# Kernel optimization log

Hardware: AMD Instinct MI355X
Metric: run time of the kernel (lower is better)

The kernel has to match this reference:

```python
import jax, jax.numpy as jnp
import numpy as np
import math

IN_DIM = 256
HID_DIM = 256
NUM_EDGE_TYPES = 3
HEADS = 8
HEAD_DIM = HID_DIM // HEADS  # 32
QK_DIM = (NUM_EDGE_TYPES + 1) * HID_DIM  # 1024
N = 4096


def _glorot(key, shape):
    # torch_geometric-style glorot: uniform(-a, a), a = sqrt(6/(fan_in+fan_out)) over last two dims
    a = math.sqrt(6.0 / (shape[-2] + shape[-1]))
    return jax.random.uniform(key, shape, jnp.float32, -a, a)


def setup_inputs() -> dict:
    key = jax.random.key(0)
    ks = jax.random.split(key, 8)
    return {
        "input_x": jax.random.normal(ks[0], (N, IN_DIM), jnp.float32),
        "pe_Q": jax.random.normal(ks[1], (N, NUM_EDGE_TYPES * HID_DIM), jnp.float32),
        "pe_K": jax.random.normal(ks[2], (N, NUM_EDGE_TYPES * HID_DIM), jnp.float32),
        "A": jnp.zeros((N, N), jnp.int32),  # accepted by forward but unused
        "WQ": _glorot(ks[3], (HEADS, QK_DIM, HEAD_DIM)),
        "WK": _glorot(ks[4], (HEADS, QK_DIM, HEAD_DIM)),
        "WV": _glorot(ks[5], (HEADS, IN_DIM, HEAD_DIM)),
        "Q_bias": jnp.zeros((HEADS, 1, HEAD_DIM), jnp.float32),
        "K_bias": jnp.zeros((HEADS, 1, HEAD_DIM), jnp.float32),
        "V_bias": jnp.zeros((HEADS, 1, HEAD_DIM), jnp.float32),
        "lin_w": _glorot(ks[6], (HID_DIM, HID_DIM)),
        "lin_b": jnp.zeros((HID_DIM,), jnp.float32),
    }


def reference(input_x, pe_Q, pe_K, A, WQ, WK, WV, Q_bias, K_bias, V_bias, lin_w, lin_b):
    x_Q = jnp.concatenate([input_x, pe_Q], axis=-1)  # [N, QK_DIM]
    x_K = jnp.concatenate([input_x, pe_K], axis=-1)  # [N, QK_DIM]
    Q = jnp.einsum('nd,hdk->hnk', x_Q, WQ) + Q_bias   # [H, N, hd]
    K = jnp.einsum('nd,hdk->hnk', x_K, WK) + K_bias   # [H, N, hd]
    V = jnp.einsum('nd,hdk->hnk', input_x, WV) + V_bias
    scores = jnp.einsum('hnk,hmk->hnm', Q, K) / math.sqrt(HID_DIM)  # [H, N, N]
    scores = scores - jax.lax.stop_gradient(jnp.max(scores, axis=-1, keepdims=True))
    attn = jax.nn.softmax(scores, axis=-1)
    attn = jnp.where(jnp.isnan(attn), jnp.zeros_like(attn), attn)
    attn_x = jnp.einsum('hnm,hmk->hnk', attn, V)      # [H, N, hd]
    # cat(list over heads, dim=1) -> [N, H*hd] with head-major column order
    x_cat = jnp.transpose(attn_x, (1, 0, 2)).reshape(attn_x.shape[1], -1)
    return x_cat @ lin_w.T + lin_b
```

## Files before the change

kernel.cpp:

```cpp
#include <hip/hip_runtime.h>
#include <hip/hip_bf16.h>

typedef __attribute__((ext_vector_type(8))) short bf16x8;
typedef __attribute__((ext_vector_type(4))) float f32x4;

#define QSCALE 0.09016844f

__device__ __forceinline__ unsigned short f2b(float f) {
    union { float f; unsigned int u; } v; v.f = f;
    unsigned int u = v.u;
    unsigned int r = (u + 0x7FFFu + ((u >> 16) & 1u)) >> 16;
    return (unsigned short)r;
}
__device__ __forceinline__ float b2f(unsigned short h) {
    union { unsigned int u; float f; } v; v.u = ((unsigned int)h) << 16;
    return v.f;
}
__device__ __forceinline__ unsigned pk2(float a, float b) {
    union { __hip_bfloat162 h; unsigned u; } c;
    c.h = __float22bfloat162_rn(make_float2(a, b));
    return c.u;
}

__global__ __launch_bounds__(256) void prep_main(
    const float* __restrict__ WQ, const float* __restrict__ WK,
    const float* __restrict__ WV, const float* __restrict__ LW,
    const float* __restrict__ Qb, const float* __restrict__ Kb,
    const float* __restrict__ Vb,
    const float* __restrict__ x, const float* __restrict__ peQ,
    const float* __restrict__ peK,
    unsigned short* __restrict__ WQt, unsigned short* __restrict__ WKt,
    unsigned short* __restrict__ WVt, unsigned short* __restrict__ LWt,
    unsigned short* __restrict__ Bq, unsigned short* __restrict__ Bk,
    unsigned short* __restrict__ Bv,
    unsigned short* __restrict__ xb, unsigned short* __restrict__ peQb,
    unsigned short* __restrict__ peKb) {
    int b = blockIdx.x, t = threadIdx.x;
    if (b < 288) {
        const float* W; unsigned short* Wt; int h, d0, D; float sc = 1.0f;
        if (b < 128)      { W = WQ; Wt = WQt; h = b >> 4;   d0 = (b & 15) * 64; D = 1024; sc = QSCALE; }
        else if (b < 256) { int bb = b - 128; W = WK; Wt = WKt; h = bb >> 4; d0 = (bb & 15) * 64; D = 1024; }
        else              { int bb = b - 256; W = WV; Wt = WVt; h = bb >> 2; d0 = (bb & 3) * 64;  D = 256; }
        __shared__ float Ts[32][65];
        int dr = t >> 2, k0 = (t & 3) * 8;
        const float* src = W + (h * D + d0 + dr) * 32 + k0;
        float4 u0 = *(const float4*)src;
        float4 u1 = *(const float4*)(src + 4);
        Ts[k0 + 0][dr] = u0.x; Ts[k0 + 1][dr] = u0.y; Ts[k0 + 2][dr] = u0.z; Ts[k0 + 3][dr] = u0.w;
        Ts[k0 + 4][dr] = u1.x; Ts[k0 + 5][dr] = u1.y; Ts[k0 + 6][dr] = u1.z; Ts[k0 + 7][dr] = u1.w;
        __syncthreads();
        int k = t >> 3, dc = (t & 7) * 8;
        union { unsigned short s[8]; uint4 v; } pk;
#pragma unroll
        for (int i = 0; i < 8; i++) pk.s[i] = f2b(Ts[k][dc + i] * sc);
        *(uint4*)(Wt + (h * 32 + k) * D + d0 + dc) = pk.v;
    } else if (b < 320) {
        int base = (b - 288) * 2048 + t * 8;
        const float* sp = LW + base;
        float4 u0 = *(const float4*)sp;
        float4 u1 = *(const float4*)(sp + 4);
        union { unsigned u[4]; uint4 v; } pk;
        pk.u[0] = pk2(u0.x, u0.y); pk.u[1] = pk2(u0.z, u0.w);
        pk.u[2] = pk2(u1.x, u1.y); pk.u[3] = pk2(u1.z, u1.w);
        *(uint4*)(LWt + base) = pk.v;
    } else if (b == 320) {
        Bq[t] = f2b(Qb[t] * QSCALE); Bk[t] = f2b(Kb[t]); Bv[t] = f2b(Vb[t]);
    } else {
        int idx = (b - 321) * 2048 + t * 8;
        const float* sp; unsigned short* dp;
        if (idx < 1048576)      { sp = x + idx;                dp = xb + idx; }
        else if (idx < 4194304) { sp = peQ + (idx - 1048576);  dp = peQb + (idx - 1048576); }
        else                    { sp = peK + (idx - 4194304);  dp = peKb + (idx - 4194304); }
        float4 u0 = *(const float4*)sp;
        float4 u1 = *(const float4*)(sp + 4);
        union { unsigned u[4]; uint4 v; } pk;
        pk.u[0] = pk2(u0.x, u0.y); pk.u[1] = pk2(u0.z, u0.w);
        pk.u[2] = pk2(u1.x, u1.y); pk.u[3] = pk2(u1.z, u1.w);
        *(uint4*)dp = pk.v;
    }
}

__global__ __launch_bounds__(256) void prep_fb(
    const float* __restrict__ WQ, const float* __restrict__ WK,
    const float* __restrict__ WV,
    const float* __restrict__ Qb, const float* __restrict__ Kb,
    const float* __restrict__ Vb,
    unsigned short* __restrict__ WQt, unsigned short* __restrict__ WKt,
    unsigned short* __restrict__ WVt,
    unsigned short* __restrict__ Bq, unsigned short* __restrict__ Bk,
    unsigned short* __restrict__ Bv) {
    int b = blockIdx.x, t = threadIdx.x;
    if (b < 288) {
        const float* W; unsigned short* Wt; int h, d0, D; float sc = 1.0f;
        if (b < 128)      { W = WQ; Wt = WQt; h = b >> 4;   d0 = (b & 15) * 64; D = 1024; sc = QSCALE; }
        else if (b < 256) { int bb = b - 128; W = WK; Wt = WKt; h = bb >> 4; d0 = (bb & 15) * 64; D = 1024; }
        else              { int bb = b - 256; W = WV; Wt = WVt; h = bb >> 2; d0 = (bb & 3) * 64;  D = 256; }
        __shared__ float Ts[32][65];
        int dr = t >> 2, k0 = (t & 3) * 8;
        const float* src = W + (h * D + d0 + dr) * 32 + k0;
        float4 u0 = *(const float4*)src;
        float4 u1 = *(const float4*)(src + 4);
        Ts[k0 + 0][dr] = u0.x; Ts[k0 + 1][dr] = u0.y; Ts[k0 + 2][dr] = u0.z; Ts[k0 + 3][dr] = u0.w;
        Ts[k0 + 4][dr] = u1.x; Ts[k0 + 5][dr] = u1.y; Ts[k0 + 6][dr] = u1.z; Ts[k0 + 7][dr] = u1.w;
        __syncthreads();
        int k = t >> 3, dc = (t & 7) * 8;
        union { unsigned short s[8]; uint4 v; } pk;
#pragma unroll
        for (int i = 0; i < 8; i++) pk.s[i] = f2b(Ts[k][dc + i] * sc);
        *(uint4*)(Wt + (h * 32 + k) * D + d0 + dc) = pk.v;
    } else {
        Bq[t] = f2b(Qb[t] * QSCALE); Bk[t] = f2b(Kb[t]); Bv[t] = f2b(Vb[t]);
    }
}

template <bool ABF16>
__global__ __launch_bounds__(256) void proj_fused(
    const void* __restrict__ xv,
    const void* __restrict__ peQv, const void* __restrict__ peKv,
    const unsigned short* __restrict__ WQt, const unsigned short* __restrict__ WKt,
    const unsigned short* __restrict__ WVt,
    const unsigned short* __restrict__ Bq, const unsigned short* __restrict__ Bk,
    const unsigned short* __restrict__ Bv,
    unsigned short* __restrict__ Qc, unsigned short* __restrict__ KV) {
    __shared__ unsigned short As[64 * 72];
    __shared__ unsigned short Bs[64 * 72];
    int bx = blockIdx.x;
    int which = bx >> 8, bb = bx & 255;
    const void* A1; const unsigned short* Bt; const unsigned short* bias; int K;
    if (which == 0)      { A1 = peQv; Bt = WQt; bias = Bq; K = 1024; }
    else if (which == 1) { A1 = peKv; Bt = WKt; bias = Bk; K = 1024; }
    else                 { A1 = peQv; Bt = WVt; bias = Bv; K = 256; }
    int mb = bb & 63, nb = bb >> 6;
    int m0 = mb * 64, n0 = nb * 64;
    int t = threadIdx.x, w = t >> 6, lane = t & 63;
    int ln = lane & 15, q8 = (lane >> 4) * 8;
    int wm = (w >> 1) * 32, wn = (w & 1) * 32;
    int sr = t >> 3, sc = (t & 7) * 8;
    f32x4 acc[2][2];
#pragma unroll
    for (int i = 0; i < 2; i++)
#pragma unroll
        for (int j = 0; j < 2; j++) acc[i][j] = (f32x4){0.f, 0.f, 0.f, 0.f};
    for (int kb = 0; kb < K; kb += 64) {
#pragma unroll
        for (int half = 0; half < 2; half++) {
            int r = sr + half * 32;
            int c = kb + sc;
            if (ABF16) {
                const unsigned short* ap = (c < 256)
                    ? ((const unsigned short*)xv + (m0 + r) * 256 + c)
                    : ((const unsigned short*)A1 + (m0 + r) * 768 + (c - 256));
                *(uint4*)&As[r * 72 + sc] = *(const uint4*)ap;
            } else {
                const float* ap = (c < 256)
                    ? ((const float*)xv + (m0 + r) * 256 + c)
                    : ((const float*)A1 + (m0 + r) * 768 + (c - 256));
                float4 u0 = *(const float4*)ap;
                float4 u1 = *(const float4*)(ap + 4);
                union { unsigned u[4]; uint4 v; } pk;
                pk.u[0] = pk2(u0.x, u0.y); pk.u[1] = pk2(u0.z, u0.w);
                pk.u[2] = pk2(u1.x, u1.y); pk.u[3] = pk2(u1.z, u1.w);
                *(uint4*)&As[r * 72 + sc] = pk.v;
            }
            *(uint4*)&Bs[r * 72 + sc] = *(const uint4*)(Bt + (n0 + r) * K + c);
        }
        __syncthreads();
#pragma unroll
        for (int ks = 0; ks < 64; ks += 32) {
            bf16x8 a[2], b[2];
#pragma unroll
            for (int i = 0; i < 2; i++) {
                a[i] = *(const bf16x8*)&As[(wm + i * 16 + ln) * 72 + ks + q8];
                b[i] = *(const bf16x8*)&Bs[(wn + i * 16 + ln) * 72 + ks + q8];
            }
#pragma unroll
            for (int i = 0; i < 2; i++)
#pragma unroll
                for (int j = 0; j < 2; j++)
                    acc[i][j] = __builtin_amdgcn_mfma_f32_16x16x32_bf16(a[i], b[j], acc[i][j], 0, 0, 0);
        }
        __syncthreads();
    }
#pragma unroll
    for (int j = 0; j < 2; j++) {
        int ncol = n0 + wn + j * 16 + ln;
        float bv = b2f(bias[ncol]);
        int h2 = ncol >> 5, din = ncol & 31;
#pragma unroll
        for (int i = 0; i < 2; i++) {
            int rbase = m0 + wm + i * 16 + ((lane >> 4) * 4);
            if (which == 0) {
#pragma unroll
                for (int r = 0; r < 4; r++)
                    Qc[(rbase + r) * 256 + ncol] = f2b(acc[i][j][r] + bv);
            } else if (which == 1) {
#pragma unroll
                for (int r = 0; r < 4; r++) {
                    int key = rbase + r;
                    int T2 = key >> 6, k6 = key & 63;
                    int kt = ((k6 >> 2) & 1) + ((k6 >> 4) & 2);
                    int ln2 = ((k6 >> 3) & 3) * 4 + (k6 & 3);
                    int addr = (h2 * 64 + T2) * 4096 + kt * 512
                             + ((din >> 3) * 16 + ln2) * 8 + (din & 7);
                    KV[addr] = f2b(acc[i][j][r] + bv);
                }
            } else {
                int key = rbase;
                int T2 = key >> 6, k6 = key & 63;
                int chunk = 4 + ((din >> 4) << 1) + ((k6 >> 5) & 1);
                int lane2 = ((k6 >> 3) & 3) * 16 + (din & 15);
                int addr = (h2 * 64 + T2) * 4096 + chunk * 512 + lane2 * 8 + (k6 & 7);
                uint2 vv;
                vv.x = pk2(acc[i][j][0] + bv, acc[i][j][1] + bv);
                vv.y = pk2(acc[i][j][2] + bv, acc[i][j][3] + bv);
                *(uint2*)(KV + addr) = vv;
            }
        }
    }
}

__global__ __launch_bounds__(512, 4) void attn_kernel(
    const unsigned short* __restrict__ Qc,
    const unsigned short* __restrict__ KV,
    unsigned short* __restrict__ Xc) {
    __shared__ float Om[8][32][65];
    __shared__ float Ls[8][64];
    int head = blockIdx.x & 7;
    int qb = blockIdx.x >> 3;
    int t = threadIdx.x, w = t >> 6, lane = t & 63;
    int ln = lane & 15, quad = lane >> 4, q8 = quad * 8;
    int q0 = qb * 64;
    bf16x8 qfv[4];
#pragma unroll
    for (int qf = 0; qf < 4; qf++)
        qfv[qf] = *(const bf16x8*)(Qc + (q0 + qf * 16 + ln) * 256 + head * 32 + q8);
    const unsigned short* kv = KV + (head * 64 + w * 8) * 4096 + lane * 8;
    f32x4 o[4][2];
    float lts[4] = {0.f, 0.f, 0.f, 0.f};
#pragma unroll
    for (int qf = 0; qf < 4; qf++)
#pragma unroll
        for (int hh = 0; hh < 2; hh++) o[qf][hh] = (f32x4){0.f, 0.f, 0.f, 0.f};
    const f32x4 z = {0.f, 0.f, 0.f, 0.f};
#pragma unroll 1
    for (int it = 0; it < 8; it++) {
        const unsigned short* ckv = kv + it * 4096;
        bf16x8 k0 = *(const bf16x8*)(ckv + 0);
        bf16x8 k1 = *(const bf16x8*)(ckv + 512);
        bf16x8 k2 = *(const bf16x8*)(ckv + 1024);
        bf16x8 k3 = *(const bf16x8*)(ckv + 1536);
        bf16x8 v0 = *(const bf16x8*)(ckv + 2048);
        bf16x8 v1 = *(const bf16x8*)(ckv + 2560);
        bf16x8 v2 = *(const bf16x8*)(ckv + 3072);
        bf16x8 v3 = *(const bf16x8*)(ckv + 3584);
#pragma unroll
        for (int qf = 0; qf < 4; qf++) {
            f32x4 s0 = __builtin_amdgcn_mfma_f32_16x16x32_bf16(k0, qfv[qf], z, 0, 0, 0);
            f32x4 s1 = __builtin_amdgcn_mfma_f32_16x16x32_bf16(k1, qfv[qf], z, 0, 0, 0);
            f32x4 s2 = __builtin_amdgcn_mfma_f32_16x16x32_bf16(k2, qfv[qf], z, 0, 0, 0);
            f32x4 s3 = __builtin_amdgcn_mfma_f32_16x16x32_bf16(k3, qfv[qf], z, 0, 0, 0);
            float p0[4], p1[4], p2[4], p3[4];
#pragma unroll
            for (int r = 0; r < 4; r++) {
                p0[r] = __builtin_amdgcn_exp2f(s0[r]);
                p1[r] = __builtin_amdgcn_exp2f(s1[r]);
                p2[r] = __builtin_amdgcn_exp2f(s2[r]);
                p3[r] = __builtin_amdgcn_exp2f(s3[r]);
            }
            float psum = 0.f;
#pragma unroll
            for (int r = 0; r < 4; r++) psum += (p0[r] + p1[r]) + (p2[r] + p3[r]);
            lts[qf] += psum;
            union { unsigned u[4]; bf16x8 v; } b0, b1;
            b0.u[0] = pk2(p0[0], p0[1]); b0.u[1] = pk2(p0[2], p0[3]);
            b0.u[2] = pk2(p1[0], p1[1]); b0.u[3] = pk2(p1[2], p1[3]);
            b1.u[0] = pk2(p2[0], p2[1]); b1.u[1] = pk2(p2[2], p2[3]);
            b1.u[2] = pk2(p3[0], p3[1]); b1.u[3] = pk2(p3[2], p3[3]);
            o[qf][0] = __builtin_amdgcn_mfma_f32_16x16x32_bf16(v0, b0.v, o[qf][0], 0, 0, 0);
            o[qf][0] = __builtin_amdgcn_mfma_f32_16x16x32_bf16(v1, b1.v, o[qf][0], 0, 0, 0);
            o[qf][1] = __builtin_amdgcn_mfma_f32_16x16x32_bf16(v2, b0.v, o[qf][1], 0, 0, 0);
            o[qf][1] = __builtin_amdgcn_mfma_f32_16x16x32_bf16(v3, b1.v, o[qf][1], 0, 0, 0);
        }
    }
#pragma unroll
    for (int qf = 0; qf < 4; qf++) {
        float l = lts[qf];
        l += __shfl_xor(l, 16, 64);
        l += __shfl_xor(l, 32, 64);
#pragma unroll
        for (int r = 0; r < 4; r++) {
            Om[w][quad * 4 + r][qf * 16 + ln] = o[qf][0][r];
            Om[w][16 + quad * 4 + r][qf * 16 + ln] = o[qf][1][r];
        }
        if (quad == 0) Ls[w][qf * 16 + ln] = l;
    }
    __syncthreads();
    int q = t & 63, d = (t >> 6) * 4;
    float num[4] = {0.f, 0.f, 0.f, 0.f};
    float den = 0.f;
#pragma unroll
    for (int w2 = 0; w2 < 8; w2++) {
        den += Ls[w2][q];
#pragma unroll
        for (int i = 0; i < 4; i++) num[i] += Om[w2][d + i][q];
    }
    float inv = 1.f / den;
    uint2 outv;
    outv.x = pk2(num[0] * inv, num[1] * inv);
    outv.y = pk2(num[2] * inv, num[3] * inv);
    *(uint2*)(Xc + (q0 + q) * 256 + head * 32 + d) = outv;
}

template <bool BBF16>
__global__ __launch_bounds__(256) void gemm_out(
    const unsigned short* __restrict__ A,
    const void* __restrict__ LWv,
    const float* __restrict__ Lb,
    float* __restrict__ C) {
    __shared__ unsigned short As[64 * 72];
    __shared__ unsigned short Bs[64 * 72];
    int mb = blockIdx.x & 63, nb = blockIdx.x >> 6;
    int m0 = mb * 64, n0 = nb * 64;
    int t = threadIdx.x, w = t >> 6, lane = t & 63;
    int ln = lane & 15, q8 = (lane >> 4) * 8;
    int wm = (w >> 1) * 32, wn = (w & 1) * 32;
    int sr = t >> 3, sc = (t & 7) * 8;
    f32x4 acc[2][2];
#pragma unroll
    for (int i = 0; i < 2; i++)
#pragma unroll
        for (int j = 0; j < 2; j++) acc[i][j] = (f32x4){0.f, 0.f, 0.f, 0.f};
    for (int kb = 0; kb < 256; kb += 64) {
#pragma unroll
        for (int half = 0; half < 2; half++) {
            int r = sr + half * 32;
            int c = kb + sc;
            *(uint4*)&As[r * 72 + sc] = *(const uint4*)(A + (m0 + r) * 256 + c);
            if (BBF16) {
                *(uint4*)&Bs[r * 72 + sc] =
                    *(const uint4*)((const unsigned short*)LWv + (n0 + r) * 256 + c);
            } else {
                const float* bp = (const float*)LWv + (n0 + r) * 256 + c;
                float4 u0 = *(const float4*)bp;
                float4 u1 = *(const float4*)(bp + 4);
                union { unsigned u[4]; uint4 v; } pk;
                pk.u[0] = pk2(u0.x, u0.y); pk.u[1] = pk2(u0.z, u0.w);
                pk.u[2] = pk2(u1.x, u1.y); pk.u[3] = pk2(u1.z, u1.w);
                *(uint4*)&Bs[r * 72 + sc] = pk.v;
            }
        }
        __syncthreads();
#pragma unroll
        for (int ks = 0; ks < 64; ks += 32) {
            bf16x8 a[2], b[2];
#pragma unroll
            for (int i = 0; i < 2; i++) {
                a[i] = *(const bf16x8*)&As[(wm + i * 16 + ln) * 72 + ks + q8];
                b[i] = *(const bf16x8*)&Bs[(wn + i * 16 + ln) * 72 + ks + q8];
            }
#pragma unroll
            for (int i = 0; i < 2; i++)
#pragma unroll
                for (int j = 0; j < 2; j++)
                    acc[i][j] = __builtin_amdgcn_mfma_f32_16x16x32_bf16(a[i], b[j], acc[i][j], 0, 0, 0);
        }
        __syncthreads();
    }
#pragma unroll
    for (int j = 0; j < 2; j++) {
        int ncol = n0 + wn + j * 16 + ln;
        float bv = Lb[ncol];
#pragma unroll
        for (int i = 0; i < 2; i++) {
            int rbase = m0 + wm + i * 16 + ((lane >> 4) * 4);
#pragma unroll
            for (int r = 0; r < 4; r++)
                C[(rbase + r) * 256 + ncol] = acc[i][j][r] + bv;
        }
    }
}

extern "C" void kernel_launch(void* const* d_in, const int* in_sizes, int n_in,
                              void* d_out, int out_size, void* d_ws, size_t ws_size,
                              hipStream_t stream) {
    const float* input_x = (const float*)d_in[0];
    const float* pe_Q    = (const float*)d_in[1];
    const float* pe_K    = (const float*)d_in[2];
    const float* WQ = (const float*)d_in[4];
    const float* WK = (const float*)d_in[5];
    const float* WV = (const float*)d_in[6];
    const float* Qb = (const float*)d_in[7];
    const float* Kb = (const float*)d_in[8];
    const float* Vb = (const float*)d_in[9];
    const float* lw = (const float*)d_in[10];
    const float* lb = (const float*)d_in[11];
    float* outp = (float*)d_out;

    unsigned short* ws = (unsigned short*)d_ws;
    unsigned short* WQt = ws;
    unsigned short* WKt = WQt + 262144;
    unsigned short* WVt = WKt + 262144;
    unsigned short* LWt = WVt + 65536;
    unsigned short* Bq  = LWt + 65536;
    unsigned short* Bk  = Bq + 256;
    unsigned short* Bv  = Bk + 256;
    unsigned short* xb   = Bv + 256;
    unsigned short* peQb = xb + 1048576;
    unsigned short* peKb = peQb + 3145728;
    unsigned short* Qc   = peKb + 3145728;
    unsigned short* KVb  = Qc + 1048576;
    unsigned short* Xc   = KVb + 2097152;
    size_t need = (size_t)(Xc + 1048576 - ws) * 2;

    if (ws_size >= need) {
        prep_main<<<dim3(3905), dim3(256), 0, stream>>>(
            WQ, WK, WV, lw, Qb, Kb, Vb, input_x, pe_Q, pe_K,
            WQt, WKt, WVt, LWt, Bq, Bk, Bv, xb, peQb, peKb);
        proj_fused<true><<<dim3(768), dim3(256), 0, stream>>>(
            xb, peQb, peKb, WQt, WKt, WVt, Bq, Bk, Bv, Qc, KVb);
        attn_kernel<<<dim3(512), dim3(512), 0, stream>>>(Qc, KVb, Xc);
        gemm_out<true><<<dim3(256), dim3(256), 0, stream>>>(Xc, LWt, lb, outp);
    } else {
        unsigned short* Qc2  = Bv + 256;
        unsigned short* KV2  = Qc2 + 1048576;
        unsigned short* Xc2  = KV2 + 2097152;
        prep_fb<<<dim3(289), dim3(256), 0, stream>>>(WQ, WK, WV, Qb, Kb, Vb,
                                                     WQt, WKt, WVt, Bq, Bk, Bv);
        proj_fused<false><<<dim3(768), dim3(256), 0, stream>>>(
            input_x, pe_Q, pe_K, WQt, WKt, WVt, Bq, Bk, Bv, Qc2, KV2);
        attn_kernel<<<dim3(512), dim3(512), 0, stream>>>(Qc2, KV2, Xc2);
        gemm_out<false><<<dim3(256), dim3(256), 0, stream>>>(Xc2, lw, lb, outp);
    }
}
```

Baseline: 182.3 us.

## Restructure attention to per-wave query rows with double-buffered LDS K/V panel

```diff
diff --git a/kernel.cpp b/kernel.cpp
--- a/kernel.cpp
+++ b/kernel.cpp
@@ -219,96 +219,87 @@
     }
 }
 
-__global__ __launch_bounds__(512, 4) void attn_kernel(
+__global__ __launch_bounds__(256, 2) void attn_kernel(
     const unsigned short* __restrict__ Qc,
     const unsigned short* __restrict__ KV,
     unsigned short* __restrict__ Xc) {
-    __shared__ float Om[8][32][65];
-    __shared__ float Ls[8][64];
+    __shared__ unsigned short Kt[2][4096];
     int head = blockIdx.x & 7;
     int qb = blockIdx.x >> 3;
-    int t = threadIdx.x, w = t >> 6, lane = t & 63;
+    int tid = threadIdx.x, w = tid >> 6, lane = tid & 63;
     int ln = lane & 15, quad = lane >> 4, q8 = quad * 8;
     int q0 = qb * 64;
-    bf16x8 qfv[4];
-#pragma unroll
-    for (int qf = 0; qf < 4; qf++)
-        qfv[qf] = *(const bf16x8*)(Qc + (q0 + qf * 16 + ln) * 256 + head * 32 + q8);
-    const unsigned short* kv = KV + (head * 64 + w * 8) * 4096 + lane * 8;
-    f32x4 o[4][2];
-    float lts[4] = {0.f, 0.f, 0.f, 0.f};
-#pragma unroll
-    for (int qf = 0; qf < 4; qf++)
-#pragma unroll
-        for (int hh = 0; hh < 2; hh++) o[qf][hh] = (f32x4){0.f, 0.f, 0.f, 0.f};
+    int qrow = q0 + w * 16 + ln;
+    bf16x8 qv = *(const bf16x8*)(Qc + qrow * 256 + head * 32 + q8);
+    bf16x8 ones;
+#pragma unroll
+    for (int i = 0; i < 8; i++) ones[i] = (short)0x3F80;
     const f32x4 z = {0.f, 0.f, 0.f, 0.f};
+    f32x4 o0 = z, o1 = z, lacc = z;
+    const unsigned short* panel = KV + head * 64 * 4096;
+    {
+        const uint4* sp = (const uint4*)panel;
+        *(uint4*)&Kt[0][tid * 16] = sp[tid * 2];
+        *(uint4*)&Kt[0][tid * 16 + 8] = sp[tid * 2 + 1];
+    }
+    __syncthreads();
 #pragma unroll 1
-    for (int it = 0; it < 8; it++) {
-        const unsigned short* ckv = kv + it * 4096;
-        bf16x8 k0 = *(const bf16x8*)(ckv + 0);
-        bf16x8 k1 = *(const bf16x8*)(ckv + 512);
-        bf16x8 k2 = *(const bf16x8*)(ckv + 1024);
-        bf16x8 k3 = *(const bf16x8*)(ckv + 1536);
-        bf16x8 v0 = *(const bf16x8*)(ckv + 2048);
-        bf16x8 v1 = *(const bf16x8*)(ckv + 2560);
-        bf16x8 v2 = *(const bf16x8*)(ckv + 3072);
-        bf16x8 v3 = *(const bf16x8*)(ckv + 3584);
-#pragma unroll
-        for (int qf = 0; qf < 4; qf++) {
-            f32x4 s0 = __builtin_amdgcn_mfma_f32_16x16x32_bf16(k0, qfv[qf], z, 0, 0, 0);
-            f32x4 s1 = __builtin_amdgcn_mfma_f32_16x16x32_bf16(k1, qfv[qf], z, 0, 0, 0);
-            f32x4 s2 = __builtin_amdgcn_mfma_f32_16x16x32_bf16(k2, qfv[qf], z, 0, 0, 0);
-            f32x4 s3 = __builtin_amdgcn_mfma_f32_16x16x32_bf16(k3, qfv[qf], z, 0, 0, 0);
-            float p0[4], p1[4], p2[4], p3[4];
-#pragma unroll
-            for (int r = 0; r < 4; r++) {
-                p0[r] = __builtin_amdgcn_exp2f(s0[r]);
-                p1[r] = __builtin_amdgcn_exp2f(s1[r]);
-                p2[r] = __builtin_amdgcn_exp2f(s2[r]);
-                p3[r] = __builtin_amdgcn_exp2f(s3[r]);
-            }
-            float psum = 0.f;
-#pragma unroll
-            for (int r = 0; r < 4; r++) psum += (p0[r] + p1[r]) + (p2[r] + p3[r]);
-            lts[qf] += psum;
-            union { unsigned u[4]; bf16x8 v; } b0, b1;
-            b0.u[0] = pk2(p0[0], p0[1]); b0.u[1] = pk2(p0[2], p0[3]);
-            b0.u[2] = pk2(p1[0], p1[1]); b0.u[3] = pk2(p1[2], p1[3]);
-            b1.u[0] = pk2(p2[0], p2[1]); b1.u[1] = pk2(p2[2], p2[3]);
-            b1.u[2] = pk2(p3[0], p3[1]); b1.u[3] = pk2(p3[2], p3[3]);
-            o[qf][0] = __builtin_amdgcn_mfma_f32_16x16x32_bf16(v0, b0.v, o[qf][0], 0, 0, 0);
-            o[qf][0] = __builtin_amdgcn_mfma_f32_16x16x32_bf16(v1, b1.v, o[qf][0], 0, 0, 0);
-            o[qf][1] = __builtin_amdgcn_mfma_f32_16x16x32_bf16(v2, b0.v, o[qf][1], 0, 0, 0);
-            o[qf][1] = __builtin_amdgcn_mfma_f32_16x16x32_bf16(v3, b1.v, o[qf][1], 0, 0, 0);
-        }
-    }
-#pragma unroll
-    for (int qf = 0; qf < 4; qf++) {
-        float l = lts[qf];
-        l += __shfl_xor(l, 16, 64);
-        l += __shfl_xor(l, 32, 64);
+    for (int it = 0; it < 64; ++it) {
+        int cur = it & 1;
+        uint4 n0, n1;
+        if (it < 63) {
+            const uint4* ns = (const uint4*)(panel + (it + 1) * 4096);
+            n0 = ns[tid * 2]; n1 = ns[tid * 2 + 1];
+        }
+        const unsigned short* kb = &Kt[cur][0];
+        bf16x8 k0 = *(const bf16x8*)(kb + lane * 8);
+        bf16x8 k1 = *(const bf16x8*)(kb + 512 + lane * 8);
+        bf16x8 k2 = *(const bf16x8*)(kb + 1024 + lane * 8);
+        bf16x8 k3 = *(const bf16x8*)(kb + 1536 + lane * 8);
+        bf16x8 v0 = *(const bf16x8*)(kb + 2048 + lane * 8);
+        bf16x8 v1 = *(const bf16x8*)(kb + 2560 + lane * 8);
+        bf16x8 v2 = *(const bf16x8*)(kb + 3072 + lane * 8);
+        bf16x8 v3 = *(const bf16x8*)(kb + 3584 + lane * 8);
+        f32x4 s0 = __builtin_amdgcn_mfma_f32_16x16x32_bf16(k0, qv, z, 0, 0, 0);
+        f32x4 s1 = __builtin_amdgcn_mfma_f32_16x16x32_bf16(k1, qv, z, 0, 0, 0);
+        f32x4 s2 = __builtin_amdgcn_mfma_f32_16x16x32_bf16(k2, qv, z, 0, 0, 0);
+        f32x4 s3 = __builtin_amdgcn_mfma_f32_16x16x32_bf16(k3, qv, z, 0, 0, 0);
+        float p0[4], p1[4], p2[4], p3[4];
 #pragma unroll
         for (int r = 0; r < 4; r++) {
-            Om[w][quad * 4 + r][qf * 16 + ln] = o[qf][0][r];
-            Om[w][16 + quad * 4 + r][qf * 16 + ln] = o[qf][1][r];
-        }
-        if (quad == 0) Ls[w][qf * 16 + ln] = l;
-    }
-    __syncthreads();
-    int q = t & 63, d = (t >> 6) * 4;
-    float num[4] = {0.f, 0.f, 0.f, 0.f};
-    float den = 0.f;
-#pragma unroll
-    for (int w2 = 0; w2 < 8; w2++) {
-        den += Ls[w2][q];
-#pragma unroll
-        for (int i = 0; i < 4; i++) num[i] += Om[w2][d + i][q];
-    }
-    float inv = 1.f / den;
-    uint2 outv;
-    outv.x = pk2(num[0] * inv, num[1] * inv);
-    outv.y = pk2(num[2] * inv, num[3] * inv);
-    *(uint2*)(Xc + (q0 + q) * 256 + head * 32 + d) = outv;
+            p0[r] = __builtin_amdgcn_exp2f(s0[r]);
+            p1[r] = __builtin_amdgcn_exp2f(s1[r]);
+            p2[r] = __builtin_amdgcn_exp2f(s2[r]);
+            p3[r] = __builtin_amdgcn_exp2f(s3[r]);
+        }
+        union { unsigned u[4]; bf16x8 v; } b0, b1;
+        b0.u[0] = pk2(p0[0], p0[1]); b0.u[1] = pk2(p0[2], p0[3]);
+        b0.u[2] = pk2(p1[0], p1[1]); b0.u[3] = pk2(p1[2], p1[3]);
+        b1.u[0] = pk2(p2[0], p2[1]); b1.u[1] = pk2(p2[2], p2[3]);
+        b1.u[2] = pk2(p3[0], p3[1]); b1.u[3] = pk2(p3[2], p3[3]);
+        lacc = __builtin_amdgcn_mfma_f32_16x16x32_bf16(ones, b0.v, lacc, 0, 0, 0);
+        lacc = __builtin_amdgcn_mfma_f32_16x16x32_bf16(ones, b1.v, lacc, 0, 0, 0);
+        o0 = __builtin_amdgcn_mfma_f32_16x16x32_bf16(v0, b0.v, o0, 0, 0, 0);
+        o0 = __builtin_amdgcn_mfma_f32_16x16x32_bf16(v1, b1.v, o0, 0, 0, 0);
+        o1 = __builtin_amdgcn_mfma_f32_16x16x32_bf16(v2, b0.v, o1, 0, 0, 0);
+        o1 = __builtin_amdgcn_mfma_f32_16x16x32_bf16(v3, b1.v, o1, 0, 0, 0);
+        __syncthreads();
+        if (it < 63) {
+            int nxt = cur ^ 1;
+            *(uint4*)&Kt[nxt][tid * 16] = n0;
+            *(uint4*)&Kt[nxt][tid * 16 + 8] = n1;
+        }
+        __syncthreads();
+    }
+    float inv = 1.f / lacc[0];
+    uint2 r0v, r1v;
+    r0v.x = pk2(o0[0] * inv, o0[1] * inv);
+    r0v.y = pk2(o0[2] * inv, o0[3] * inv);
+    r1v.x = pk2(o1[0] * inv, o1[1] * inv);
+    r1v.y = pk2(o1[2] * inv, o1[3] * inv);
+    unsigned short* xp = Xc + qrow * 256 + head * 32 + quad * 4;
+    *(uint2*)(xp) = r0v;
+    *(uint2*)(xp + 16) = r1v;
 }
 
 template <bool BBF16>
@@ -418,7 +409,7 @@
             WQt, WKt, WVt, LWt, Bq, Bk, Bv, xb, peQb, peKb);
         proj_fused<true><<<dim3(768), dim3(256), 0, stream>>>(
             xb, peQb, peKb, WQt, WKt, WVt, Bq, Bk, Bv, Qc, KVb);
-        attn_kernel<<<dim3(512), dim3(512), 0, stream>>>(Qc, KVb, Xc);
+        attn_kernel<<<dim3(512), dim3(256), 0, stream>>>(Qc, KVb, Xc);
         gemm_out<true><<<dim3(256), dim3(256), 0, stream>>>(Xc, LWt, lb, outp);
     } else {
         unsigned short* Qc2  = Bv + 256;
@@ -428,7 +419,7 @@
                                                      WQt, WKt, WVt, Bq, Bk, Bv);
         proj_fused<false><<<dim3(768), dim3(256), 0, stream>>>(
             input_x, pe_Q, pe_K, WQt, WKt, WVt, Bq, Bk, Bv, Qc2, KV2);
-        attn_kernel<<<dim3(512), dim3(512), 0, stream>>>(Qc2, KV2, Xc2);
+        attn_kernel<<<dim3(512), dim3(256), 0, stream>>>(Qc2, KV2, Xc2);
         gemm_out<false><<<dim3(256), dim3(256), 0, stream>>>(Xc2, lw, lb, outp);
     }
 }
```

Result: slower. 190.3 us (+4.4%).

## Double-buffer KV loads in attention and compute row sums with MFMA

Applied to the files above, without the earlier changes.

```diff
diff --git a/kernel.cpp b/kernel.cpp
--- a/kernel.cpp
+++ b/kernel.cpp
@@ -219,7 +219,37 @@
     }
 }
 
-__global__ __launch_bounds__(512, 4) void attn_kernel(
+#define TILE_COMPUTE(K0_, K1_, K2_, K3_, V0_, V1_, V2_, V3_)                          \
+    do {                                                                              \
+        _Pragma("unroll")                                                             \
+        for (int qf = 0; qf < 4; qf++) {                                              \
+            f32x4 s0 = __builtin_amdgcn_mfma_f32_16x16x32_bf16(K0_, qfv[qf], z, 0, 0, 0); \
+            f32x4 s1 = __builtin_amdgcn_mfma_f32_16x16x32_bf16(K1_, qfv[qf], z, 0, 0, 0); \
+            f32x4 s2 = __builtin_amdgcn_mfma_f32_16x16x32_bf16(K2_, qfv[qf], z, 0, 0, 0); \
+            f32x4 s3 = __builtin_amdgcn_mfma_f32_16x16x32_bf16(K3_, qfv[qf], z, 0, 0, 0); \
+            float p0[4], p1[4], p2[4], p3[4];                                         \
+            _Pragma("unroll")                                                         \
+            for (int r = 0; r < 4; r++) {                                             \
+                p0[r] = __builtin_amdgcn_exp2f(s0[r]);                                \
+                p1[r] = __builtin_amdgcn_exp2f(s1[r]);                                \
+                p2[r] = __builtin_amdgcn_exp2f(s2[r]);                                \
+                p3[r] = __builtin_amdgcn_exp2f(s3[r]);                                \
+            }                                                                         \
+            union { unsigned u[4]; bf16x8 v; } pa, pb;                                \
+            pa.u[0] = pk2(p0[0], p0[1]); pa.u[1] = pk2(p0[2], p0[3]);                 \
+            pa.u[2] = pk2(p1[0], p1[1]); pa.u[3] = pk2(p1[2], p1[3]);                 \
+            pb.u[0] = pk2(p2[0], p2[1]); pb.u[1] = pk2(p2[2], p2[3]);                 \
+            pb.u[2] = pk2(p3[0], p3[1]); pb.u[3] = pk2(p3[2], p3[3]);                 \
+            lacc[qf] = __builtin_amdgcn_mfma_f32_16x16x32_bf16(ones, pa.v, lacc[qf], 0, 0, 0); \
+            lacc[qf] = __builtin_amdgcn_mfma_f32_16x16x32_bf16(ones, pb.v, lacc[qf], 0, 0, 0); \
+            o[qf][0] = __builtin_amdgcn_mfma_f32_16x16x32_bf16(V0_, pa.v, o[qf][0], 0, 0, 0); \
+            o[qf][0] = __builtin_amdgcn_mfma_f32_16x16x32_bf16(V1_, pb.v, o[qf][0], 0, 0, 0); \
+            o[qf][1] = __builtin_amdgcn_mfma_f32_16x16x32_bf16(V2_, pa.v, o[qf][1], 0, 0, 0); \
+            o[qf][1] = __builtin_amdgcn_mfma_f32_16x16x32_bf16(V3_, pb.v, o[qf][1], 0, 0, 0); \
+        }                                                                             \
+    } while (0)
+
+__global__ __launch_bounds__(512, 2) void attn_kernel(
     const unsigned short* __restrict__ Qc,
     const unsigned short* __restrict__ KV,
     unsigned short* __restrict__ Xc) {
@@ -235,80 +265,74 @@
     for (int qf = 0; qf < 4; qf++)
         qfv[qf] = *(const bf16x8*)(Qc + (q0 + qf * 16 + ln) * 256 + head * 32 + q8);
     const unsigned short* kv = KV + (head * 64 + w * 8) * 4096 + lane * 8;
+    bf16x8 ones;
+#pragma unroll
+    for (int i = 0; i < 8; i++) ones[i] = (short)0x3F80;
+    const f32x4 z = {0.f, 0.f, 0.f, 0.f};
     f32x4 o[4][2];
-    float lts[4] = {0.f, 0.f, 0.f, 0.f};
-#pragma unroll
-    for (int qf = 0; qf < 4; qf++)
-#pragma unroll
-        for (int hh = 0; hh < 2; hh++) o[qf][hh] = (f32x4){0.f, 0.f, 0.f, 0.f};
-    const f32x4 z = {0.f, 0.f, 0.f, 0.f};
+    f32x4 lacc[4];
+#pragma unroll
+    for (int qf = 0; qf < 4; qf++) {
+        o[qf][0] = z; o[qf][1] = z; lacc[qf] = z;
+    }
+    bf16x8 ta0 = *(const bf16x8*)(kv + 0);
+    bf16x8 ta1 = *(const bf16x8*)(kv + 512);
+    bf16x8 ta2 = *(const bf16x8*)(kv + 1024);
+    bf16x8 ta3 = *(const bf16x8*)(kv + 1536);
+    bf16x8 ta4 = *(const bf16x8*)(kv + 2048);
+    bf16x8 ta5 = *(const bf16x8*)(kv + 2560);
+    bf16x8 ta6 = *(const bf16x8*)(kv + 3072);
+    bf16x8 ta7 = *(const bf16x8*)(kv + 3584);
 #pragma unroll 1
-    for (int it = 0; it < 8; it++) {
-        const unsigned short* ckv = kv + it * 4096;
-        bf16x8 k0 = *(const bf16x8*)(ckv + 0);
-        bf16x8 k1 = *(const bf16x8*)(ckv + 512);
-        bf16x8 k2 = *(const bf16x8*)(ckv + 1024);
-        bf16x8 k3 = *(const bf16x8*)(ckv + 1536);
-        bf16x8 v0 = *(const bf16x8*)(ckv + 2048);
-        bf16x8 v1 = *(const bf16x8*)(ckv + 2560);
-        bf16x8 v2 = *(const bf16x8*)(ckv + 3072);
-        bf16x8 v3 = *(const bf16x8*)(ckv + 3584);
-#pragma unroll
-        for (int qf = 0; qf < 4; qf++) {
-            f32x4 s0 = __builtin_amdgcn_mfma_f32_16x16x32_bf16(k0, qfv[qf], z, 0, 0, 0);
-            f32x4 s1 = __builtin_amdgcn_mfma_f32_16x16x32_bf16(k1, qfv[qf], z, 0, 0, 0);
-            f32x4 s2 = __builtin_amdgcn_mfma_f32_16x16x32_bf16(k2, qfv[qf], z, 0, 0, 0);
-            f32x4 s3 = __builtin_amdgcn_mfma_f32_16x16x32_bf16(k3, qfv[qf], z, 0, 0, 0);
-            float p0[4], p1[4], p2[4], p3[4];
-#pragma unroll
-            for (int r = 0; r < 4; r++) {
-                p0[r] = __builtin_amdgcn_exp2f(s0[r]);
-                p1[r] = __builtin_amdgcn_exp2f(s1[r]);
-                p2[r] = __builtin_amdgcn_exp2f(s2[r]);
-                p3[r] = __builtin_amdgcn_exp2f(s3[r]);
-            }
-            float psum = 0.f;
-#pragma unroll
-            for (int r = 0; r < 4; r++) psum += (p0[r] + p1[r]) + (p2[r] + p3[r]);
-            lts[qf] += psum;
-            union { unsigned u[4]; bf16x8 v; } b0, b1;
-            b0.u[0] = pk2(p0[0], p0[1]); b0.u[1] = pk2(p0[2], p0[3]);
-            b0.u[2] = pk2(p1[0], p1[1]); b0.u[3] = pk2(p1[2], p1[3]);
-            b1.u[0] = pk2(p2[0], p2[1]); b1.u[1] = pk2(p2[2], p2[3]);
-            b1.u[2] = pk2(p3[0], p3[1]); b1.u[3] = pk2(p3[2], p3[3]);
-            o[qf][0] = __builtin_amdgcn_mfma_f32_16x16x32_bf16(v0, b0.v, o[qf][0], 0, 0, 0);
-            o[qf][0] = __builtin_amdgcn_mfma_f32_16x16x32_bf16(v1, b1.v, o[qf][0], 0, 0, 0);
-            o[qf][1] = __builtin_amdgcn_mfma_f32_16x16x32_bf16(v2, b0.v, o[qf][1], 0, 0, 0);
-            o[qf][1] = __builtin_amdgcn_mfma_f32_16x16x32_bf16(v3, b1.v, o[qf][1], 0, 0, 0);
-        }
+    for (int it = 0; it < 8; it += 2) {
+        const unsigned short* pB = kv + (it + 1) * 4096;
+        bf16x8 tb0 = *(const bf16x8*)(pB + 0);
+        bf16x8 tb1 = *(const bf16x8*)(pB + 512);
+        bf16x8 tb2 = *(const bf16x8*)(pB + 1024);
+        bf16x8 tb3 = *(const bf16x8*)(pB + 1536);
+        bf16x8 tb4 = *(const bf16x8*)(pB + 2048);
+        bf16x8 tb5 = *(const bf16x8*)(pB + 2560);
+        bf16x8 tb6 = *(const bf16x8*)(pB + 3072);
+        bf16x8 tb7 = *(const bf16x8*)(pB + 3584);
+        __builtin_amdgcn_sched_barrier(0);
+        TILE_COMPUTE(ta0, ta1, ta2, ta3, ta4, ta5, ta6, ta7);
+        int nit2 = (it + 2 < 8) ? (it + 2) : 7;
+        const unsigned short* pA = kv + nit2 * 4096;
+        ta0 = *(const bf16x8*)(pA + 0);
+        ta1 = *(const bf16x8*)(pA + 512);
+        ta2 = *(const bf16x8*)(pA + 1024);
+        ta3 = *(const bf16x8*)(pA + 1536);
+        ta4 = *(const bf16x8*)(pA + 2048);
+        ta5 = *(const bf16x8*)(pA + 2560);
+        ta6 = *(const bf16x8*)(pA + 3072);
+        ta7 = *(const bf16x8*)(pA + 3584);
+        __builtin_amdgcn_sched_barrier(0);
+        TILE_COMPUTE(tb0, tb1, tb2, tb3, tb4, tb5, tb6, tb7);
     }
 #pragma unroll
     for (int qf = 0; qf < 4; qf++) {
-        float l = lts[qf];
-        l += __shfl_xor(l, 16, 64);
-        l += __shfl_xor(l, 32, 64);
 #pragma unroll
         for (int r = 0; r < 4; r++) {
             Om[w][quad * 4 + r][qf * 16 + ln] = o[qf][0][r];
             Om[w][16 + quad * 4 + r][qf * 16 + ln] = o[qf][1][r];
         }
-        if (quad == 0) Ls[w][qf * 16 + ln] = l;
+        if (quad == 0) Ls[w][qf * 16 + ln] = lacc[qf][0];
     }
     __syncthreads();
-    int q = t & 63, d = (t >> 6) * 4;
+    int q6 = t & 63, d = (t >> 6) * 4;
     float num[4] = {0.f, 0.f, 0.f, 0.f};
     float den = 0.f;
 #pragma unroll
     for (int w2 = 0; w2 < 8; w2++) {
-        den += Ls[w2][q];
-#pragma unroll
-        for (int i = 0; i < 4; i++) num[i] += Om[w2][d + i][q];
+        den += Ls[w2][q6];
+#pragma unroll
+        for (int i = 0; i < 4; i++) num[i] += Om[w2][d + i][q6];
     }
     float inv = 1.f / den;
     uint2 outv;
     outv.x = pk2(num[0] * inv, num[1] * inv);
     outv.y = pk2(num[2] * inv, num[3] * inv);
-    *(uint2*)(Xc + (q0 + q) * 256 + head * 32 + d) = outv;
+    *(uint2*)(Xc + (q0 + q6) * 256 + head * 32 + d) = outv;
 }
 
 template <bool BBF16>
```

Result: faster. 177.1 us (-2.8%).
